# Kernel optimization log

Measured on AMD Instinct MI355X. Metric: run time of the kernel, lower is better.

Reference implementation:

```python
import jax, jax.numpy as jnp
import numpy as np

NUM_HEADS = 8
NUM_GROUPS = 32  # min(32, channels=256)
EPS = 1e-5


def group_norm(x, w, b):
    # x: [B, C, L]
    B, C, L = x.shape
    xg = x.reshape(B, NUM_GROUPS, C // NUM_GROUPS, L)
    mu = xg.mean(axis=(2, 3), keepdims=True)
    var = xg.var(axis=(2, 3), keepdims=True)
    xn = ((xg - mu) * jax.lax.rsqrt(var + EPS)).reshape(B, C, L)
    return xn * w[None, :, None] + b[None, :, None]


def setup_inputs() -> dict:
    key = jax.random.key(0)
    ks = jax.random.split(key, 5)
    B, C, L = 4, 256, 2048
    x = jax.random.normal(ks[0], (B, C, L), dtype=jnp.float32)
    gn_w = jnp.ones((C,), dtype=jnp.float32)
    gn_b = jnp.zeros((C,), dtype=jnp.float32)
    qkv_w = jax.random.normal(ks[1], (3 * C, C), dtype=jnp.float32) * (C ** -0.5)
    qkv_b = jax.random.normal(ks[2], (3 * C,), dtype=jnp.float32) * 0.02
    out_w = jax.random.normal(ks[3], (C, C), dtype=jnp.float32) * (C ** -0.5)
    out_b = jax.random.normal(ks[4], (C,), dtype=jnp.float32) * 0.02
    return {"x": x, "gn_w": gn_w, "gn_b": gn_b, "qkv_w": qkv_w,
            "qkv_b": qkv_b, "out_w": out_w, "out_b": out_b}


def reference(x, gn_w, gn_b, qkv_w, qkv_b, out_w, out_b):
    B, C, L = x.shape
    H = NUM_HEADS
    D = C // H
    h = group_norm(x, gn_w, gn_b)
    # 1x1 conv == channel matmul: [B,3C,L]
    qkv = jnp.einsum('oc,bcl->bol', qkv_w, h) + qkv_b[None, :, None]
    qkv = qkv.reshape(B, 3, H, D, L)
    q, k, v = qkv[:, 0], qkv[:, 1], qkv[:, 2]  # each [B,H,D,L]
    scale = D ** -0.5
    attn = jnp.einsum('bhdn,bhdm->bhnm', q * scale, k)  # [B,H,L,L]
    attn = jax.nn.softmax(attn, axis=-1)
    h = jnp.einsum('bhnm,bhdm->bhdn', attn, v).reshape(B, C, L)
    out = jnp.einsum('oc,bcl->bol', out_w, h) + out_b[None, :, None]
    return x + out
```

## Files before the change

### kernel.cpp

```cpp
#include <hip/hip_runtime.h>
#include <math.h>

using f32x4  = __attribute__((ext_vector_type(4))) float;
using bf16x8 = __attribute__((ext_vector_type(8))) short;

constexpr int kB = 4, kC = 256, kL = 2048, kH = 8;
constexpr float kQScale = 0.25505402264f;

__device__ __forceinline__ unsigned short f2bf(float f) {
    unsigned u = __builtin_bit_cast(unsigned, f);
    u += 0x7fffu + ((u >> 16) & 1u);
    return (unsigned short)(u >> 16);
}
__device__ __forceinline__ unsigned cvt_pk(float lo, float hi) {
    unsigned r;
    asm("v_cvt_pk_bf16_f32 %0, %1, %2" : "=v"(r) : "v"(lo), "v"(hi));
    return r;
}
__device__ __forceinline__ f32x4 mfma16(bf16x8 a, bf16x8 b, f32x4 c) {
    return __builtin_amdgcn_mfma_f32_16x16x32_bf16(a, b, c, 0, 0, 0);
}
__device__ __forceinline__ bf16x8 bc8(unsigned a, unsigned b, unsigned c, unsigned d) {
    return __builtin_bit_cast(bf16x8, make_uint4(a, b, c, d));
}
__device__ __forceinline__ void glds16(const unsigned short* g, unsigned short* l) {
    __builtin_amdgcn_global_load_lds(
        (const __attribute__((address_space(1))) unsigned int*)g,
        (__attribute__((address_space(3))) unsigned int*)l, 16, 0, 0);
}

__global__ __launch_bounds__(256) void gncvt_kernel(const float* __restrict__ x,
                                                    const float* __restrict__ gw,
                                                    const float* __restrict__ gb,
                                                    unsigned short* __restrict__ hT,
                                                    const float* __restrict__ qkvw,
                                                    const float* __restrict__ outw,
                                                    unsigned short* __restrict__ wq,
                                                    unsigned short* __restrict__ wo) {
    if (blockIdx.x >= 128) {
        int i = (blockIdx.x - 128) * 256 + threadIdx.x;
        const float* s; unsigned short* d; int j;
        if (i < 49152) { s = qkvw; d = wq; j = i; }
        else           { s = outw; d = wo; j = i - 49152; }
        float4 v = ((const float4*)s)[j];
        ((uint2*)d)[j] = make_uint2(cvt_pk(v.x, v.y), cvt_pk(v.z, v.w));
        return;
    }
    int b = blockIdx.x >> 5, g = blockIdx.x & 31;
    int t = threadIdx.x;
    const float* xp = x + ((size_t)b * kC + g * 8) * kL + 8 * t;

    float v[8][8];
    float s = 0.f, ss = 0.f;
#pragma unroll
    for (int c = 0; c < 8; ++c) {
        float4 a  = *(const float4*)(xp + (size_t)c * kL);
        float4 a2 = *(const float4*)(xp + (size_t)c * kL + 4);
        v[c][0]=a.x; v[c][1]=a.y; v[c][2]=a.z; v[c][3]=a.w;
        v[c][4]=a2.x; v[c][5]=a2.y; v[c][6]=a2.z; v[c][7]=a2.w;
        s  += (a.x+a.y)+(a.z+a.w)+(a2.x+a2.y)+(a2.z+a2.w);
        ss += a.x*a.x+a.y*a.y+a.z*a.z+a.w*a.w+a2.x*a2.x+a2.y*a2.y+a2.z*a2.z+a2.w*a2.w;
    }
#pragma unroll
    for (int off = 32; off; off >>= 1) {
        s  += __shfl_down(s, off);
        ss += __shfl_down(ss, off);
    }
    __shared__ float red[8];
    int wv = t >> 6;
    if ((t & 63) == 0) { red[wv] = s; red[4 + wv] = ss; }
    __syncthreads();
    s  = red[0] + red[1] + red[2] + red[3];
    ss = red[4] + red[5] + red[6] + red[7];
    float mean = s * (1.f / 16384.f);
    float var  = ss * (1.f / 16384.f) - mean * mean;
    float rstd = rsqrtf(var + 1e-5f);

    float wc[8], bc[8];
#pragma unroll
    for (int c = 0; c < 8; ++c) { wc[c] = gw[g*8+c] * rstd; bc[c] = gb[g*8+c]; }

    unsigned short* hp = hT + ((size_t)b * kL + 8 * t) * kC + g * 8;
#pragma unroll
    for (int j = 0; j < 8; ++j) {
        unsigned pk[4];
#pragma unroll
        for (int c2 = 0; c2 < 4; ++c2) {
            pk[c2] = cvt_pk((v[2*c2  ][j] - mean) * wc[2*c2  ] + bc[2*c2  ],
                            (v[2*c2+1][j] - mean) * wc[2*c2+1] + bc[2*c2+1]);
        }
        *(uint4*)(hp + (size_t)j * kC) = make_uint4(pk[0], pk[1], pk[2], pk[3]);
    }
}

__device__ __forceinline__ void store_qk(unsigned short* __restrict__ base, size_t bh,
                                         int n, int d0, f32x4 acc,
                                         const float* bias4, float scale) {
    float v0 = (acc[0] + bias4[0]) * scale, v1 = (acc[1] + bias4[1]) * scale;
    float v2 = (acc[2] + bias4[2]) * scale, v3 = (acc[3] + bias4[3]) * scale;
    *(uint2*)(base + (bh * kL + n) * 32 + d0) = make_uint2(cvt_pk(v0, v1), cvt_pk(v2, v3));
}

__global__ __launch_bounds__(256) void qkv_gemm(const unsigned short* __restrict__ Wb,
                                                const unsigned short* __restrict__ hT,
                                                const float* __restrict__ qkvb,
                                                unsigned short* __restrict__ qT,
                                                unsigned short* __restrict__ kT,
                                                unsigned short* __restrict__ vbuf) {
    __shared__ alignas(16) unsigned short Hlds[2][8][512];
    int t = threadIdx.x, wv = t >> 6, ll = t & 15, lg = (t >> 4) & 3;
    int lane = t & 63;
    int n0 = blockIdx.x * 128, o0 = blockIdx.y * 64, b = blockIdx.z;
    int obase = o0 + wv * 16;
    const unsigned short* hb = hT + (size_t)b * kL * kC;

    bf16x8 wf[8];
#pragma unroll
    for (int k = 0; k < 8; ++k)
        wf[k] = *(const bf16x8*)(Wb + (size_t)(obase + ll) * 256 + 32 * k + 8 * lg);
    float bias[4];
#pragma unroll
    for (int r = 0; r < 4; ++r) bias[r] = qkvb[obase + 4 * lg + r];
    int mode = (obase < 256) ? 0 : (obase < 512 ? 1 : 2);
    int d0 = (obase & 31) + 4 * lg;

    const unsigned short* hsrc0 = hb + (size_t)(n0 + 16 * (2 * wv)     + ll) * 256 + 8 * lg;
    const unsigned short* hsrc1 = hb + (size_t)(n0 + 16 * (2 * wv + 1) + ll) * 256 + 8 * lg;

    glds16(hsrc0,      &Hlds[0][2 * wv][0]);
    glds16(hsrc1,      &Hlds[0][2 * wv + 1][0]);
    glds16(hsrc0 + 32, &Hlds[1][2 * wv][0]);
    glds16(hsrc1 + 32, &Hlds[1][2 * wv + 1][0]);
    asm volatile("s_waitcnt vmcnt(2)" ::: "memory");
    __builtin_amdgcn_sched_barrier(0);
    __builtin_amdgcn_s_barrier();

    f32x4 acc[8] = {};
    int cur = 0;
    for (int c = 0; c < 8; ++c) {
        bf16x8 hf[8];
#pragma unroll
        for (int nj = 0; nj < 8; ++nj)
            hf[nj] = *(const bf16x8*)&Hlds[cur][nj][lane * 8];
        asm volatile("s_waitcnt lgkmcnt(0)" ::: "memory");
        __builtin_amdgcn_sched_barrier(0);
        __builtin_amdgcn_s_barrier();

        int kn = ((c + 2) & 7) * 32;
        glds16(hsrc0 + kn, &Hlds[cur][2 * wv][0]);
        glds16(hsrc1 + kn, &Hlds[cur][2 * wv + 1][0]);

        __builtin_amdgcn_s_setprio(1);
#pragma unroll
        for (int nj = 0; nj < 8; ++nj)
            acc[nj] = mfma16(wf[c], hf[nj], acc[nj]);
        __builtin_amdgcn_s_setprio(0);

        asm volatile("s_waitcnt vmcnt(2)" ::: "memory");
        __builtin_amdgcn_sched_barrier(0);
        __builtin_amdgcn_s_barrier();
        cur ^= 1;
    }
    asm volatile("s_waitcnt vmcnt(0)" ::: "memory");

#pragma unroll
    for (int nj = 0; nj < 8; ++nj) {
        int n = n0 + 16 * nj + ll;
        if (mode == 0) {
            store_qk(qT, (size_t)b * kH + (obase >> 5), n, d0, acc[nj], bias, kQScale);
        } else if (mode == 1) {
            store_qk(kT, (size_t)b * kH + ((obase - 256) >> 5), n, d0, acc[nj], bias, 1.f);
        } else {
#pragma unroll
            for (int r = 0; r < 4; ++r) {
                size_t row = (size_t)b * kC + (obase - 512) + 4 * lg + r;
                vbuf[row * kL + n] = f2bf(acc[nj][r] + bias[r]);
            }
        }
    }
}

__global__ __launch_bounds__(256) void attn_kernel(const unsigned short* __restrict__ qT,
                                                   const unsigned short* __restrict__ kT,
                                                   const unsigned short* __restrict__ vbuf,
                                                   unsigned short* __restrict__ h2T) {
    __shared__ alignas(16) unsigned short Klds[2][4][512];
    __shared__ alignas(16) unsigned short Vlds[2][4][512];
    __shared__ unsigned Plds[4][32][34];
    int t = threadIdx.x, wv = t >> 6, ll = t & 15, hi = (t >> 4) & 3;
    int lane = t & 63;
    int j = blockIdx.x;
    int bid = (j & 7) * 64 + (j >> 3);
    int qg = bid & 15, bh = bid >> 4;
    int b = bh >> 3, h = bh & 7;
    const unsigned short* qb = qT + (size_t)bh * kL * 32;
    const unsigned short* kb = kT + (size_t)bh * kL * 32;
    const unsigned short* vb = vbuf + ((size_t)b * kC + h * 32) * kL;
    int nbase = qg * 128 + wv * 32;

    bf16x8 qf[2];
#pragma unroll
    for (int nj = 0; nj < 2; ++nj)
        qf[nj] = *(const bf16x8*)(qb + (size_t)(nbase + 16 * nj + ll) * 32 + 8 * hi);

    f32x4 acc[2][2] = {};
    float lsum[2] = {0.f, 0.f};
    const f32x4 zero = {0.f, 0.f, 0.f, 0.f};

    const unsigned short* ksrc = kb + (size_t)(16 * wv + ll) * 32 + 8 * hi;
    const unsigned short* vsrc = vb + (size_t)(16 * (wv >> 1) + ll) * kL + 32 * (wv & 1) + 8 * hi;

    glds16(ksrc, &Klds[0][wv][0]);
    glds16(vsrc, &Vlds[0][wv][0]);
    glds16(ksrc + (size_t)64 * 32, &Klds[1][wv][0]);
    glds16(vsrc + 64,              &Vlds[1][wv][0]);
    asm volatile("s_waitcnt vmcnt(2)" ::: "memory");
    __builtin_amdgcn_sched_barrier(0);
    __builtin_amdgcn_s_barrier();

    int cur = 0;
    for (int it = 0; it < 32; ++it) {
        bf16x8 ka[4], va[2][2];
#pragma unroll
        for (int mj = 0; mj < 4; ++mj)
            ka[mj] = *(const bf16x8*)&Klds[cur][mj][lane * 8];
#pragma unroll
        for (int dj = 0; dj < 2; ++dj)
#pragma unroll
            for (int tt = 0; tt < 2; ++tt)
                va[dj][tt] = *(const bf16x8*)&Vlds[cur][dj * 2 + tt][lane * 8];

        asm volatile("s_waitcnt lgkmcnt(0)" ::: "memory");
        __builtin_amdgcn_sched_barrier(0);
        __builtin_amdgcn_s_barrier();

        int kn = ((it + 2) & 31) * 64;
        glds16(ksrc + (size_t)kn * 32, &Klds[cur][wv][0]);
        glds16(vsrc + kn,              &Vlds[cur][wv][0]);

        f32x4 s[4][2];
        __builtin_amdgcn_s_setprio(1);
#pragma unroll
        for (int mj = 0; mj < 4; ++mj)
#pragma unroll
            for (int nj = 0; nj < 2; ++nj)
                s[mj][nj] = mfma16(ka[mj], qf[nj], zero);
        __builtin_amdgcn_s_setprio(0);

#pragma unroll
        for (int mj = 0; mj < 4; ++mj)
#pragma unroll
            for (int nj = 0; nj < 2; ++nj) {
                float p0 = __builtin_amdgcn_exp2f(s[mj][nj][0]);
                float p1 = __builtin_amdgcn_exp2f(s[mj][nj][1]);
                float p2 = __builtin_amdgcn_exp2f(s[mj][nj][2]);
                float p3 = __builtin_amdgcn_exp2f(s[mj][nj][3]);
                lsum[nj] += (p0 + p1) + (p2 + p3);
                *(uint2*)&Plds[wv][16 * nj + ll][8 * mj + 2 * hi] =
                    make_uint2(cvt_pk(p0, p1), cvt_pk(p2, p3));
            }

        bf16x8 pbf[2][2];
#pragma unroll
        for (int nj = 0; nj < 2; ++nj)
#pragma unroll
            for (int tt = 0; tt < 2; ++tt) {
                uint2 lo  = *(uint2*)&Plds[wv][16 * nj + ll][16 * tt + 4 * hi];
                uint2 hi2 = *(uint2*)&Plds[wv][16 * nj + ll][16 * tt + 4 * hi + 2];
                pbf[nj][tt] = bc8(lo.x, lo.y, hi2.x, hi2.y);
            }

        __builtin_amdgcn_s_setprio(1);
#pragma unroll
        for (int tt = 0; tt < 2; ++tt)
#pragma unroll
            for (int nj = 0; nj < 2; ++nj)
#pragma unroll
                for (int dj = 0; dj < 2; ++dj)
                    acc[nj][dj] = mfma16(va[dj][tt], pbf[nj][tt], acc[nj][dj]);
        __builtin_amdgcn_s_setprio(0);

        asm volatile("s_waitcnt vmcnt(2)" ::: "memory");
        __builtin_amdgcn_sched_barrier(0);
        __builtin_amdgcn_s_barrier();
        cur ^= 1;
    }
    asm volatile("s_waitcnt vmcnt(0)" ::: "memory");

#pragma unroll
    for (int nj = 0; nj < 2; ++nj) {
        lsum[nj] += __shfl_xor(lsum[nj], 16);
        lsum[nj] += __shfl_xor(lsum[nj], 32);
        float inv = 1.f / lsum[nj];
        unsigned short* ob = h2T + ((size_t)b * kL + nbase + 16 * nj + ll) * kC + h * 32;
#pragma unroll
        for (int dj = 0; dj < 2; ++dj) {
            *(uint2*)(ob + 16 * dj + 4 * hi) =
                make_uint2(cvt_pk(acc[nj][dj][0] * inv, acc[nj][dj][1] * inv),
                           cvt_pk(acc[nj][dj][2] * inv, acc[nj][dj][3] * inv));
        }
    }
}

__global__ __launch_bounds__(256) void out_gemm(const unsigned short* __restrict__ Wb,
                                                const unsigned short* __restrict__ h2T,
                                                const float* __restrict__ outb,
                                                const float* __restrict__ x,
                                                float* __restrict__ out) {
    __shared__ alignas(16) unsigned short Hlds[2][8][512];
    int t = threadIdx.x, wv = t >> 6, ll = t & 15, lg = (t >> 4) & 3;
    int lane = t & 63;
    int n0 = blockIdx.x * 128, o0 = blockIdx.y * 64, b = blockIdx.z;
    int obase = o0 + wv * 16;
    const unsigned short* hb = h2T + (size_t)b * kL * kC;

    bf16x8 wf[8];
#pragma unroll
    for (int k = 0; k < 8; ++k)
        wf[k] = *(const bf16x8*)(Wb + (size_t)(obase + ll) * 256 + 32 * k + 8 * lg);
    float bias[4];
#pragma unroll
    for (int r = 0; r < 4; ++r) bias[r] = outb[obase + 4 * lg + r];

    const unsigned short* hsrc0 = hb + (size_t)(n0 + 16 * (2 * wv)     + ll) * 256 + 8 * lg;
    const unsigned short* hsrc1 = hb + (size_t)(n0 + 16 * (2 * wv + 1) + ll) * 256 + 8 * lg;

    glds16(hsrc0,      &Hlds[0][2 * wv][0]);
    glds16(hsrc1,      &Hlds[0][2 * wv + 1][0]);
    glds16(hsrc0 + 32, &Hlds[1][2 * wv][0]);
    glds16(hsrc1 + 32, &Hlds[1][2 * wv + 1][0]);
    asm volatile("s_waitcnt vmcnt(2)" ::: "memory");
    __builtin_amdgcn_sched_barrier(0);
    __builtin_amdgcn_s_barrier();

    f32x4 acc[8] = {};
    int cur = 0;
    for (int c = 0; c < 8; ++c) {
        bf16x8 hf[8];
#pragma unroll
        for (int nj = 0; nj < 8; ++nj)
            hf[nj] = *(const bf16x8*)&Hlds[cur][nj][lane * 8];
        asm volatile("s_waitcnt lgkmcnt(0)" ::: "memory");
        __builtin_amdgcn_sched_barrier(0);
        __builtin_amdgcn_s_barrier();

        int kn = ((c + 2) & 7) * 32;
        glds16(hsrc0 + kn, &Hlds[cur][2 * wv][0]);
        glds16(hsrc1 + kn, &Hlds[cur][2 * wv + 1][0]);

        __builtin_amdgcn_s_setprio(1);
#pragma unroll
        for (int nj = 0; nj < 8; ++nj)
            acc[nj] = mfma16(wf[c], hf[nj], acc[nj]);
        __builtin_amdgcn_s_setprio(0);

        asm volatile("s_waitcnt vmcnt(2)" ::: "memory");
        __builtin_amdgcn_sched_barrier(0);
        __builtin_amdgcn_s_barrier();
        cur ^= 1;
    }
    asm volatile("s_waitcnt vmcnt(0)" ::: "memory");

#pragma unroll
    for (int nj = 0; nj < 8; ++nj) {
        int n = n0 + 16 * nj + ll;
#pragma unroll
        for (int r = 0; r < 4; ++r) {
            size_t row = (size_t)b * kC + obase + 4 * lg + r;
            out[row * kL + n] = acc[nj][r] + bias[r] + x[row * kL + n];
        }
    }
}

extern "C" void kernel_launch(void* const* d_in, const int* in_sizes, int n_in,
                              void* d_out, int out_size, void* d_ws, size_t ws_size,
                              hipStream_t stream) {
    const float* x     = (const float*)d_in[0];
    const float* gn_w  = (const float*)d_in[1];
    const float* gn_b  = (const float*)d_in[2];
    const float* qkv_w = (const float*)d_in[3];
    const float* qkv_b = (const float*)d_in[4];
    const float* out_w = (const float*)d_in[5];
    const float* out_b = (const float*)d_in[6];
    float* out = (float*)d_out;

    char* ws = (char*)d_ws;
    const size_t MB = 1024 * 1024;
    unsigned short* hT   = (unsigned short*)(ws);
    unsigned short* qT   = (unsigned short*)(ws + 4  * MB);
    unsigned short* kT   = (unsigned short*)(ws + 8  * MB);
    unsigned short* vbuf = (unsigned short*)(ws + 12 * MB);
    unsigned short* h2T  = (unsigned short*)(ws + 16 * MB);
    unsigned short* wqkv = (unsigned short*)(ws + 20 * MB);
    unsigned short* wout = (unsigned short*)(ws + 20 * MB + 512 * 1024);

    gncvt_kernel<<<dim3(384), 256, 0, stream>>>(x, gn_w, gn_b, hT, qkv_w, out_w, wqkv, wout);
    qkv_gemm<<<dim3(16, 12, kB), 256, 0, stream>>>(wqkv, hT, qkv_b, qT, kT, vbuf);
    attn_kernel<<<dim3(512), 256, 0, stream>>>(qT, kT, vbuf, h2T);
    out_gemm<<<dim3(16, 4, kB), 256, 0, stream>>>(wout, h2T, out_b, x, out);
}
```

Baseline: 74.95 us.

## Halve attention query tile per wave and double attention grid

Each wave in the attention kernel now processes 16 query rows instead of 32, so a block covers 64 queries and the grid grows from 512 to 1024 blocks. The aim is more parallelism and lower per-wave register and LDS pressure, with more waves in flight on the 256 CUs. In exchange every K/V tile is loaded from global memory and LDS twice as often per query, which lowers data reuse and raises the ratio of loads and barriers to MFMA work.

```diff
diff --git a/kernel.cpp b/kernel.cpp
--- a/kernel.cpp
+++ b/kernel.cpp
@@ -186,25 +186,22 @@
                                                    unsigned short* __restrict__ h2T) {
     __shared__ alignas(16) unsigned short Klds[2][4][512];
     __shared__ alignas(16) unsigned short Vlds[2][4][512];
-    __shared__ unsigned Plds[4][32][34];
+    __shared__ unsigned Plds[4][16][34];
     int t = threadIdx.x, wv = t >> 6, ll = t & 15, hi = (t >> 4) & 3;
     int lane = t & 63;
     int j = blockIdx.x;
-    int bid = (j & 7) * 64 + (j >> 3);
-    int qg = bid & 15, bh = bid >> 4;
+    int bid = (j & 7) * 128 + (j >> 3);
+    int qg = bid & 31, bh = bid >> 5;
     int b = bh >> 3, h = bh & 7;
     const unsigned short* qb = qT + (size_t)bh * kL * 32;
     const unsigned short* kb = kT + (size_t)bh * kL * 32;
     const unsigned short* vb = vbuf + ((size_t)b * kC + h * 32) * kL;
-    int nbase = qg * 128 + wv * 32;
-
-    bf16x8 qf[2];
-#pragma unroll
-    for (int nj = 0; nj < 2; ++nj)
-        qf[nj] = *(const bf16x8*)(qb + (size_t)(nbase + 16 * nj + ll) * 32 + 8 * hi);
-
-    f32x4 acc[2][2] = {};
-    float lsum[2] = {0.f, 0.f};
+    int nq = qg * 64 + wv * 16;
+
+    bf16x8 qf = *(const bf16x8*)(qb + (size_t)(nq + ll) * 32 + 8 * hi);
+
+    f32x4 acc[2] = {};
+    float lsum = 0.f;
     const f32x4 zero = {0.f, 0.f, 0.f, 0.f};
 
     const unsigned short* ksrc = kb + (size_t)(16 * wv + ll) * 32 + 8 * hi;
@@ -238,46 +235,38 @@
         glds16(ksrc + (size_t)kn * 32, &Klds[cur][wv][0]);
         glds16(vsrc + kn,              &Vlds[cur][wv][0]);
 
-        f32x4 s[4][2];
+        f32x4 s[4];
         __builtin_amdgcn_s_setprio(1);
 #pragma unroll
         for (int mj = 0; mj < 4; ++mj)
-#pragma unroll
-            for (int nj = 0; nj < 2; ++nj)
-                s[mj][nj] = mfma16(ka[mj], qf[nj], zero);
+            s[mj] = mfma16(ka[mj], qf, zero);
         __builtin_amdgcn_s_setprio(0);
 
 #pragma unroll
-        for (int mj = 0; mj < 4; ++mj)
-#pragma unroll
-            for (int nj = 0; nj < 2; ++nj) {
-                float p0 = __builtin_amdgcn_exp2f(s[mj][nj][0]);
-                float p1 = __builtin_amdgcn_exp2f(s[mj][nj][1]);
-                float p2 = __builtin_amdgcn_exp2f(s[mj][nj][2]);
-                float p3 = __builtin_amdgcn_exp2f(s[mj][nj][3]);
-                lsum[nj] += (p0 + p1) + (p2 + p3);
-                *(uint2*)&Plds[wv][16 * nj + ll][8 * mj + 2 * hi] =
-                    make_uint2(cvt_pk(p0, p1), cvt_pk(p2, p3));
-            }
-
-        bf16x8 pbf[2][2];
-#pragma unroll
-        for (int nj = 0; nj < 2; ++nj)
-#pragma unroll
-            for (int tt = 0; tt < 2; ++tt) {
-                uint2 lo  = *(uint2*)&Plds[wv][16 * nj + ll][16 * tt + 4 * hi];
-                uint2 hi2 = *(uint2*)&Plds[wv][16 * nj + ll][16 * tt + 4 * hi + 2];
-                pbf[nj][tt] = bc8(lo.x, lo.y, hi2.x, hi2.y);
-            }
+        for (int mj = 0; mj < 4; ++mj) {
+            float p0 = __builtin_amdgcn_exp2f(s[mj][0]);
+            float p1 = __builtin_amdgcn_exp2f(s[mj][1]);
+            float p2 = __builtin_amdgcn_exp2f(s[mj][2]);
+            float p3 = __builtin_amdgcn_exp2f(s[mj][3]);
+            lsum += (p0 + p1) + (p2 + p3);
+            *(uint2*)&Plds[wv][ll][8 * mj + 2 * hi] =
+                make_uint2(cvt_pk(p0, p1), cvt_pk(p2, p3));
+        }
+
+        bf16x8 pbf[2];
+#pragma unroll
+        for (int tt = 0; tt < 2; ++tt) {
+            uint2 lo  = *(uint2*)&Plds[wv][ll][16 * tt + 4 * hi];
+            uint2 hi2 = *(uint2*)&Plds[wv][ll][16 * tt + 4 * hi + 2];
+            pbf[tt] = bc8(lo.x, lo.y, hi2.x, hi2.y);
+        }
 
         __builtin_amdgcn_s_setprio(1);
 #pragma unroll
         for (int tt = 0; tt < 2; ++tt)
 #pragma unroll
-            for (int nj = 0; nj < 2; ++nj)
-#pragma unroll
-                for (int dj = 0; dj < 2; ++dj)
-                    acc[nj][dj] = mfma16(va[dj][tt], pbf[nj][tt], acc[nj][dj]);
+            for (int dj = 0; dj < 2; ++dj)
+                acc[dj] = mfma16(va[dj][tt], pbf[tt], acc[dj]);
         __builtin_amdgcn_s_setprio(0);
 
         asm volatile("s_waitcnt vmcnt(2)" ::: "memory");
@@ -287,19 +276,14 @@
     }
     asm volatile("s_waitcnt vmcnt(0)" ::: "memory");
 
-#pragma unroll
-    for (int nj = 0; nj < 2; ++nj) {
-        lsum[nj] += __shfl_xor(lsum[nj], 16);
-        lsum[nj] += __shfl_xor(lsum[nj], 32);
-        float inv = 1.f / lsum[nj];
-        unsigned short* ob = h2T + ((size_t)b * kL + nbase + 16 * nj + ll) * kC + h * 32;
-#pragma unroll
-        for (int dj = 0; dj < 2; ++dj) {
-            *(uint2*)(ob + 16 * dj + 4 * hi) =
-                make_uint2(cvt_pk(acc[nj][dj][0] * inv, acc[nj][dj][1] * inv),
-                           cvt_pk(acc[nj][dj][2] * inv, acc[nj][dj][3] * inv));
-        }
-    }
+    lsum += __shfl_xor(lsum, 16);
+    lsum += __shfl_xor(lsum, 32);
+    float inv = 1.f / lsum;
+    unsigned short* ob = h2T + ((size_t)b * kL + nq + ll) * kC + h * 32;
+    *(uint2*)(ob + 4 * hi)      = make_uint2(cvt_pk(acc[0][0] * inv, acc[0][1] * inv),
+                                             cvt_pk(acc[0][2] * inv, acc[0][3] * inv));
+    *(uint2*)(ob + 16 + 4 * hi) = make_uint2(cvt_pk(acc[1][0] * inv, acc[1][1] * inv),
+                                             cvt_pk(acc[1][2] * inv, acc[1][3] * inv));
 }
 
 __global__ __launch_bounds__(256) void out_gemm(const unsigned short* __restrict__ Wb,
@@ -396,6 +380,6 @@
 
     gncvt_kernel<<<dim3(384), 256, 0, stream>>>(x, gn_w, gn_b, hT, qkv_w, out_w, wqkv, wout);
     qkv_gemm<<<dim3(16, 12, kB), 256, 0, stream>>>(wqkv, hT, qkv_b, qT, kT, vbuf);
-    attn_kernel<<<dim3(512), 256, 0, stream>>>(qT, kT, vbuf, h2T);
+    attn_kernel<<<dim3(1024), 256, 0, stream>>>(qT, kT, vbuf, h2T);
     out_gemm<<<dim3(16, 4, kB), 256, 0, stream>>>(wout, h2T, out_b, x, out);
 }
```

New measurement: 71.34 us. 4.8% less time.

## Split attention over key halves with a separate combine kernel; read V directly from global

Applied to the files above, without the earlier changes.

The attention kernel now splits the key/value range into two halves, which doubles the grid to 1024 blocks. Each block writes unnormalized fp32 partial accumulators and row sums to workspace, and a new combine kernel adds the two halves, normalizes, and writes the bf16 output. V is no longer staged through LDS and is loaded straight from global memory into registers. The aim is more parallelism and occupancy across CUs. The cost is extra global traffic for the partials, an extra kernel launch, and possibly less efficient V loads. It relies on the softmax having no max subtraction, so the two partial sums can be added directly.

```diff
diff --git a/kernel.cpp b/kernel.cpp
--- a/kernel.cpp
+++ b/kernel.cpp
@@ -183,20 +183,23 @@
 __global__ __launch_bounds__(256) void attn_kernel(const unsigned short* __restrict__ qT,
                                                    const unsigned short* __restrict__ kT,
                                                    const unsigned short* __restrict__ vbuf,
-                                                   unsigned short* __restrict__ h2T) {
+                                                   float* __restrict__ pacc,
+                                                   float* __restrict__ plsum) {
     __shared__ alignas(16) unsigned short Klds[2][4][512];
-    __shared__ alignas(16) unsigned short Vlds[2][4][512];
     __shared__ unsigned Plds[4][32][34];
     int t = threadIdx.x, wv = t >> 6, ll = t & 15, hi = (t >> 4) & 3;
     int lane = t & 63;
     int j = blockIdx.x;
-    int bid = (j & 7) * 64 + (j >> 3);
-    int qg = bid & 15, bh = bid >> 4;
+    int bid = (j & 7) * 128 + (j >> 3);
+    int kh = bid & 1;
+    int qg = (bid >> 1) & 15;
+    int bh = bid >> 5;
     int b = bh >> 3, h = bh & 7;
     const unsigned short* qb = qT + (size_t)bh * kL * 32;
     const unsigned short* kb = kT + (size_t)bh * kL * 32;
     const unsigned short* vb = vbuf + ((size_t)b * kC + h * 32) * kL;
     int nbase = qg * 128 + wv * 32;
+    int kstart = kh * 1024;
 
     bf16x8 qf[2];
 #pragma unroll
@@ -207,36 +210,37 @@
     float lsum[2] = {0.f, 0.f};
     const f32x4 zero = {0.f, 0.f, 0.f, 0.f};
 
-    const unsigned short* ksrc = kb + (size_t)(16 * wv + ll) * 32 + 8 * hi;
-    const unsigned short* vsrc = vb + (size_t)(16 * (wv >> 1) + ll) * kL + 32 * (wv & 1) + 8 * hi;
+    const unsigned short* ksrc = kb + (size_t)(kstart + 16 * wv + ll) * 32 + 8 * hi;
+    const int voff0 = ll * kL + 8 * hi;
+    const int voff1 = (16 + ll) * kL + 8 * hi;
 
     glds16(ksrc, &Klds[0][wv][0]);
-    glds16(vsrc, &Vlds[0][wv][0]);
     glds16(ksrc + (size_t)64 * 32, &Klds[1][wv][0]);
-    glds16(vsrc + 64,              &Vlds[1][wv][0]);
-    asm volatile("s_waitcnt vmcnt(2)" ::: "memory");
+    asm volatile("s_waitcnt vmcnt(1)" ::: "memory");
     __builtin_amdgcn_sched_barrier(0);
     __builtin_amdgcn_s_barrier();
 
     int cur = 0;
-    for (int it = 0; it < 32; ++it) {
-        bf16x8 ka[4], va[2][2];
+    for (int it = 0; it < 16; ++it) {
+        int m0 = kstart + it * 64;
+
+        bf16x8 ka[4];
 #pragma unroll
         for (int mj = 0; mj < 4; ++mj)
             ka[mj] = *(const bf16x8*)&Klds[cur][mj][lane * 8];
-#pragma unroll
-        for (int dj = 0; dj < 2; ++dj)
-#pragma unroll
-            for (int tt = 0; tt < 2; ++tt)
-                va[dj][tt] = *(const bf16x8*)&Vlds[cur][dj * 2 + tt][lane * 8];
 
         asm volatile("s_waitcnt lgkmcnt(0)" ::: "memory");
         __builtin_amdgcn_sched_barrier(0);
         __builtin_amdgcn_s_barrier();
 
-        int kn = ((it + 2) & 31) * 64;
-        glds16(ksrc + (size_t)kn * 32, &Klds[cur][wv][0]);
-        glds16(vsrc + kn,              &Vlds[cur][wv][0]);
+        bf16x8 va[2][2];
+#pragma unroll
+        for (int tt = 0; tt < 2; ++tt) {
+            va[0][tt] = *(const bf16x8*)(vb + voff0 + m0 + 32 * tt);
+            va[1][tt] = *(const bf16x8*)(vb + voff1 + m0 + 32 * tt);
+        }
+        int kn = kstart + ((it + 2) & 15) * 64;
+        glds16(kb + (size_t)(kn + 16 * wv + ll) * 32 + 8 * hi, &Klds[cur][wv][0]);
 
         f32x4 s[4][2];
         __builtin_amdgcn_s_setprio(1);
@@ -280,25 +284,50 @@
                     acc[nj][dj] = mfma16(va[dj][tt], pbf[nj][tt], acc[nj][dj]);
         __builtin_amdgcn_s_setprio(0);
 
-        asm volatile("s_waitcnt vmcnt(2)" ::: "memory");
+        asm volatile("s_waitcnt vmcnt(1)" ::: "memory");
         __builtin_amdgcn_sched_barrier(0);
         __builtin_amdgcn_s_barrier();
         cur ^= 1;
     }
     asm volatile("s_waitcnt vmcnt(0)" ::: "memory");
 
+    int qt = qg * 4 + wv;
+    int w = (bh * 64 + qt) * 2 + kh;
+    float* pa = pacc + (size_t)w * 1024;
 #pragma unroll
     for (int nj = 0; nj < 2; ++nj) {
+#pragma unroll
+        for (int dj = 0; dj < 2; ++dj)
+            *(f32x4*)(pa + (16 * nj + ll) * 32 + 16 * dj + 4 * hi) = acc[nj][dj];
         lsum[nj] += __shfl_xor(lsum[nj], 16);
         lsum[nj] += __shfl_xor(lsum[nj], 32);
-        float inv = 1.f / lsum[nj];
-        unsigned short* ob = h2T + ((size_t)b * kL + nbase + 16 * nj + ll) * kC + h * 32;
-#pragma unroll
-        for (int dj = 0; dj < 2; ++dj) {
-            *(uint2*)(ob + 16 * dj + 4 * hi) =
-                make_uint2(cvt_pk(acc[nj][dj][0] * inv, acc[nj][dj][1] * inv),
-                           cvt_pk(acc[nj][dj][2] * inv, acc[nj][dj][3] * inv));
-        }
+        if (hi == 0) plsum[w * 32 + 16 * nj + ll] = lsum[nj];
+    }
+}
+
+__global__ __launch_bounds__(256) void attn_combine(const float* __restrict__ pacc,
+                                                    const float* __restrict__ plsum,
+                                                    unsigned short* __restrict__ h2T) {
+    int idx = blockIdx.x * 256 + threadIdx.x;
+    int bh = idx >> 11, rem = idx & 2047;
+    int b = bh >> 3, h = bh & 7;
+    int qt = rem >> 5, q = rem & 31;
+    int w0 = (bh * 64 + qt) * 2;
+    const float* a0 = pacc + (size_t)w0 * 1024 + q * 32;
+    const float* a1 = a0 + 1024;
+    float inv = 1.f / (plsum[w0 * 32 + q] + plsum[w0 * 32 + 32 + q]);
+    unsigned short* ob = h2T + ((size_t)b * kL + rem) * kC + h * 32;
+#pragma unroll
+    for (int dd = 0; dd < 4; ++dd) {
+        float4 x0 = *(const float4*)(a0 + dd * 8);
+        float4 x1 = *(const float4*)(a1 + dd * 8);
+        float4 y0 = *(const float4*)(a0 + dd * 8 + 4);
+        float4 y1 = *(const float4*)(a1 + dd * 8 + 4);
+        *(uint4*)(ob + dd * 8) = make_uint4(
+            cvt_pk((x0.x + x1.x) * inv, (x0.y + x1.y) * inv),
+            cvt_pk((x0.z + x1.z) * inv, (x0.w + x1.w) * inv),
+            cvt_pk((y0.x + y1.x) * inv, (y0.y + y1.y) * inv),
+            cvt_pk((y0.z + y1.z) * inv, (y0.w + y1.w) * inv));
     }
 }
 
@@ -393,9 +422,12 @@
     unsigned short* h2T  = (unsigned short*)(ws + 16 * MB);
     unsigned short* wqkv = (unsigned short*)(ws + 20 * MB);
     unsigned short* wout = (unsigned short*)(ws + 20 * MB + 512 * 1024);
+    float* pacc  = (float*)(ws + 21 * MB);
+    float* plsum = (float*)(ws + 37 * MB);
 
     gncvt_kernel<<<dim3(384), 256, 0, stream>>>(x, gn_w, gn_b, hT, qkv_w, out_w, wqkv, wout);
     qkv_gemm<<<dim3(16, 12, kB), 256, 0, stream>>>(wqkv, hT, qkv_b, qT, kT, vbuf);
-    attn_kernel<<<dim3(512), 256, 0, stream>>>(qT, kT, vbuf, h2T);
+    attn_kernel<<<dim3(1024), 256, 0, stream>>>(qT, kT, vbuf, pacc, plsum);
+    attn_combine<<<dim3(256), 256, 0, stream>>>(pacc, plsum, h2T);
     out_gemm<<<dim3(16, 4, kB), 256, 0, stream>>>(wout, h2T, out_b, x, out);
 }
```

Measured after the change: 89.62 us. 1.2x slower.
